# Optimization experiments

Hardware: AMD Instinct MI355X
Metric: run time of the kernel (lower is better)

## Reference

```python
import jax, jax.numpy as jnp
import numpy as np

B, C, H, W = 4, 64, 128, 128
NUM_HEAD = 1
SCALE = (C // NUM_HEAD) ** (-0.5)


def setup_inputs():
    key = jax.random.key(0)
    ks = jax.random.split(key, 32)
    def nrm(k, shape, s=0.05):
        return jax.random.normal(k, shape, jnp.float32) * s
    inp = {"x": jax.random.normal(ks[0], (B, C, H, W), jnp.float32)}
    i = 1
    for wn, bn in [("Wq", "bq"), ("Wk", "bk"), ("Wv", "bv"), ("Wl", "bl"), ("Wo", "bo"), ("Wp", "bp")]:
        inp[wn] = nrm(ks[i], (C, C)); i += 1
        inp[bn] = nrm(ks[i], (C,)); i += 1
    inp["sch_dw"] = nrm(ks[i], (C, 1, 5, 1)); i += 1
    inp["sch_dwb"] = nrm(ks[i], (C,)); i += 1
    inp["sch_pw"] = nrm(ks[i], (C, C, 1, 1)); i += 1
    inp["sch_pwb"] = nrm(ks[i], (C,)); i += 1
    inp["scv_dw"] = nrm(ks[i], (C, 1, 1, 5)); i += 1
    inp["scv_dwb"] = nrm(ks[i], (C,)); i += 1
    inp["scv_pw"] = nrm(ks[i], (C, C, 1, 1)); i += 1
    inp["scv_pwb"] = nrm(ks[i], (C,)); i += 1
    inp["convh_w"] = nrm(ks[i], (C, C, 1, 1)); i += 1
    inp["convh_b"] = nrm(ks[i], (C,)); i += 1
    inp["dsc_dw"] = nrm(ks[i], (C, 1, 3, 3)); i += 1
    inp["dsc_dwb"] = nrm(ks[i], (C,)); i += 1
    inp["dsc_pw"] = nrm(ks[i], (C, C, 1, 1)); i += 1
    inp["dsc_pwb"] = nrm(ks[i], (C,)); i += 1
    inp["ln_g"] = jnp.ones((C,), jnp.float32)
    inp["ln_b"] = jnp.zeros((C,), jnp.float32)
    return inp


def _linear(x, w, b):  # x [B,N,C], w [C,C] (torch Linear convention: y = x @ w.T + b)
    return x @ w.T + b


def _dwconv(x, w, b, pad):  # depthwise: x [B,C,H,W], w [C,1,kh,kw]
    y = jax.lax.conv_general_dilated(x, w, (1, 1), [(pad[0], pad[0]), (pad[1], pad[1])],
                                     dimension_numbers=("NCHW", "OIHW", "NCHW"),
                                     feature_group_count=x.shape[1])
    return y + b[None, :, None, None]


def _pwconv(x, w, b):  # 1x1 conv: w [Co,Ci,1,1]
    return jnp.einsum("bchw,oc->bohw", x, w[:, :, 0, 0]) + b[None, :, None, None]


def _attn(q, k, v):  # [B,N,C] each; dense NxN softmax attention
    a = jax.nn.softmax(jnp.einsum("bnc,bmc->bnm", q, k) * SCALE, axis=-1)
    return jnp.einsum("bnm,bmc->bnc", a, v)


def _up2_bilinear(x):  # bilinear, scale 2, align_corners=True
    Bb, Cc, Hh, Ww = x.shape
    def coords(n):
        s = jnp.linspace(0.0, n - 1.0, 2 * n)
        i0 = jnp.floor(s).astype(jnp.int32)
        i1 = jnp.minimum(i0 + 1, n - 1)
        return i0, i1, (s - i0).astype(x.dtype)
    y0, y1, wy = coords(Hh)
    x0, x1, wx = coords(Ww)
    r = x[:, :, y0, :] * (1.0 - wy)[None, None, :, None] + x[:, :, y1, :] * wy[None, None, :, None]
    return r[:, :, :, x0] * (1.0 - wx) + r[:, :, :, x1] * wx


def _forward(x, Wq, bq, Wk, bk, Wv, bv, Wl, bl, Wo, bo, Wp, bp,
             sch_dw, sch_dwb, sch_pw, sch_pwb, scv_dw, scv_dwb, scv_pw, scv_pwb,
             convh_w, convh_b, dsc_dw, dsc_dwb, dsc_pw, dsc_pwb, ln_g, ln_b):
    Bb, Cc, Hh, Ww = x.shape
    # AvgPool2d(2,2)
    xp = x.reshape(Bb, Cc, Hh // 2, 2, Ww // 2, 2).mean((3, 5))
    Hp, Wp_ = Hh // 2, Ww // 2
    N = Hp * Wp_
    # forward_lpg: GAP-gated self-attention producing low-freq prompt
    gap = xp.mean((2, 3), keepdims=True)
    xg = (gap * xp).reshape(Bb, Cc, N).transpose(0, 2, 1)  # [B,N,C]
    q = _linear(xg, Wq, bq); k = _linear(xg, Wk, bk); v = _linear(xg, Wv, bv)
    prompt_l = _linear(_attn(q, k, v), Wl, bl).transpose(0, 2, 1).reshape(Bb, Cc, Hp, Wp_)
    # forward_hpg: separable strip-conv branches -> high-freq prompt
    x_h = _pwconv(jax.nn.gelu(_dwconv(xp, sch_dw, sch_dwb, (2, 0)), approximate=False), sch_pw, sch_pwb)
    x_v = _pwconv(jax.nn.gelu(_dwconv(xp, scv_dw, scv_dwb, (0, 2)), approximate=False), scv_pw, scv_pwb)
    prompt_h = _pwconv(x_h + x_v, convh_w, convh_b)
    # forward_pgc: cross-attention Q=high, K=low, V=linear(x)
    x_V = _linear(xp.reshape(Bb, Cc, N).transpose(0, 2, 1), Wo, bo)
    x_K = prompt_l.reshape(Bb, Cc, N).transpose(0, 2, 1)
    x_Q = prompt_h.reshape(Bb, Cc, N).transpose(0, 2, 1)
    prompt = _attn(x_Q, x_K, x_V)
    prompt = _linear(prompt, Wp, bp) + x_V
    # LayerNorm over channel dim
    mu = prompt.mean(-1, keepdims=True)
    var = jnp.mean((prompt - mu) ** 2, axis=-1, keepdims=True)
    p_norm = (prompt - mu) / jnp.sqrt(var + 1e-5) * ln_g + ln_b
    p_norm = p_norm.transpose(0, 2, 1).reshape(Bb, Cc, Hp, Wp_)
    # dsc: depthwise 3x3 -> GELU -> 1x1, residual
    out = _pwconv(jax.nn.gelu(_dwconv(p_norm, dsc_dw, dsc_dwb, (1, 1)), approximate=False), dsc_pw, dsc_pwb) + p_norm
    return _up2_bilinear(out)


def reference(x, Wq, bq, Wk, bk, Wv, bv, Wl, bl, Wo, bo, Wp, bp,
              sch_dw, sch_dwb, sch_pw, sch_pwb, scv_dw, scv_dwb, scv_pw, scv_pwb,
              convh_w, convh_b, dsc_dw, dsc_dwb, dsc_pw, dsc_pwb, ln_g, ln_b):
    return _forward(x, Wq, bq, Wk, bk, Wv, bv, Wl, bl, Wo, bo, Wp, bp,
                    sch_dw, sch_dwb, sch_pw, sch_pwb, scv_dw, scv_dwb, scv_pw, scv_pwb,
                    convh_w, convh_b, dsc_dw, dsc_dwb, dsc_pw, dsc_pwb, ln_g, ln_b)
```

## Files before the change

### kernel.cpp

```cpp
#include <hip/hip_runtime.h>
#include <math.h>

#define Bn 4
#define Cn 64
#define Np 4096
#define NSPLIT 4
#define SCALE2 0.18033688011112042f

typedef unsigned short ushort_t;
typedef __attribute__((ext_vector_type(4))) float f32x4;
typedef __attribute__((ext_vector_type(8))) short bf16x8;
typedef __attribute__((ext_vector_type(4))) short bf16x4;

__device__ __forceinline__ float gelu_exact(float x) {
    return 0.5f * x * (1.0f + erff(x * 0.70710678118654752440f));
}
__device__ __forceinline__ ushort_t f2bf(float f) {
    unsigned int u = __float_as_uint(f);
    u += 0x7fffu + ((u >> 16) & 1u);
    return (ushort_t)(u >> 16);
}
__device__ __forceinline__ ushort_t f2bf_tr(float f) {
    return (ushort_t)(__float_as_uint(f) >> 16);
}
__device__ __forceinline__ float bf2f(ushort_t h) {
    return __uint_as_float(((unsigned int)h) << 16);
}
__device__ __forceinline__ void gload_lds16(const ushort_t* g, ushort_t* l) {
    __builtin_amdgcn_global_load_lds(
        (const __attribute__((address_space(1))) void*)g,
        (__attribute__((address_space(3))) void*)l, 16, 0, 0);
}
__device__ __forceinline__ bf16x8 cvt8(const float v[8]) {
    bf16x8 r;
    #pragma unroll
    for (int j = 0; j < 8; ++j) r[j] = (short)f2bf(v[j]);
    return r;
}
__device__ __forceinline__ void gemm16b(const bf16x8 af[2], const ushort_t* __restrict__ Wb,
                                        int l16, int quad, f32x4* acc) {
    #pragma unroll
    for (int cb = 0; cb < 4; ++cb) {
        #pragma unroll
        for (int ks = 0; ks < 2; ++ks) {
            bf16x8 bw = *(const bf16x8*)(Wb + (cb * 16 + l16) * 64 + ks * 32 + quad * 8);
            acc[cb] = __builtin_amdgcn_mfma_f32_16x16x32_bf16(af[ks], bw, acc[cb], 0, 0, 0);
        }
    }
}
__device__ __forceinline__ void gemm16Tb(const bf16x8 af[2], const ushort_t* __restrict__ Wb,
                                         int l16, int quad, f32x4* acc) {
    #pragma unroll
    for (int cb = 0; cb < 4; ++cb) {
        #pragma unroll
        for (int ks = 0; ks < 2; ++ks) {
            bf16x8 bw = *(const bf16x8*)(Wb + (cb * 16 + l16) * 64 + ks * 32 + quad * 8);
            acc[cb] = __builtin_amdgcn_mfma_f32_16x16x32_bf16(bw, af[ks], acc[cb], 0, 0, 0);
        }
    }
}
__device__ __forceinline__ void aload(const float* xs, int row, int quad, bf16x8 af[2]) {
    #pragma unroll
    for (int ks = 0; ks < 2; ++ks) {
        float v[8];
        #pragma unroll
        for (int j = 0; j < 8; ++j) v[j] = xs[(ks * 32 + quad * 8 + j) * 65 + row];
        af[ks] = cvt8(v);
    }
}
__device__ __forceinline__ void stage_bchw(const float* __restrict__ X, int b, int n0, int t,
                                           float* xs) {
    #pragma unroll
    for (int u = 0; u < 16; ++u) {
        int idx = t + u * 256;
        int c = idx >> 6, nl = idx & 63;
        xs[c * 65 + nl] = X[((size_t)(b * Cn + c)) * Np + n0 + nl];
    }
}
__device__ __forceinline__ void stage_comb(const ushort_t* __restrict__ OpB, const float* linv,
                                           int b, int n0, int t, float* xs) {
    const size_t SS = (size_t)Bn * Np * Cn;
    int c4 = (t & 15) * 4;
    #pragma unroll
    for (int u = 0; u < 4; ++u) {
        int nl = (t >> 4) + u * 16;
        size_t gi = ((size_t)(b * Np + n0 + nl)) * Cn + c4;
        ushort4 a0 = *(const ushort4*)(OpB + gi);
        ushort4 a1 = *(const ushort4*)(OpB + SS + gi);
        ushort4 a2 = *(const ushort4*)(OpB + 2 * SS + gi);
        ushort4 a3 = *(const ushort4*)(OpB + 3 * SS + gi);
        float li = linv[nl];
        xs[(c4 + 0) * 65 + nl] = (bf2f(a0.x) + bf2f(a1.x) + bf2f(a2.x) + bf2f(a3.x)) * li;
        xs[(c4 + 1) * 65 + nl] = (bf2f(a0.y) + bf2f(a1.y) + bf2f(a2.y) + bf2f(a3.y)) * li;
        xs[(c4 + 2) * 65 + nl] = (bf2f(a0.z) + bf2f(a1.z) + bf2f(a2.z) + bf2f(a3.z)) * li;
        xs[(c4 + 3) * 65 + nl] = (bf2f(a0.w) + bf2f(a1.w) + bf2f(a2.w) + bf2f(a3.w)) * li;
    }
}
__device__ __forceinline__ void store_bnc_T(ushort_t* __restrict__ Y, int b, int n, int quad,
                                            const f32x4* acc, const float* __restrict__ bias,
                                            float mult) {
    #pragma unroll
    for (int cb = 0; cb < 4; ++cb) {
        int o0 = cb * 16 + quad * 4;
        ushort4 pk;
        pk.x = f2bf((acc[cb][0] + bias[o0 + 0]) * mult);
        pk.y = f2bf((acc[cb][1] + bias[o0 + 1]) * mult);
        pk.z = f2bf((acc[cb][2] + bias[o0 + 2]) * mult);
        pk.w = f2bf((acc[cb][3] + bias[o0 + 3]) * mult);
        *(ushort4*)(Y + ((size_t)(b * Np + n)) * Cn + o0) = pk;
    }
}
__device__ __forceinline__ void store_bchw_bf16(ushort_t* __restrict__ Y, int b, int nb, int l16,
                                                const f32x4* acc, const float* __restrict__ bias) {
    #pragma unroll
    for (int cb = 0; cb < 4; ++cb) {
        int col = cb * 16 + l16;
        float bb = bias[col];
        ushort4 pk;
        pk.x = f2bf(acc[cb][0] + bb); pk.y = f2bf(acc[cb][1] + bb);
        pk.z = f2bf(acc[cb][2] + bb); pk.w = f2bf(acc[cb][3] + bb);
        *(ushort4*)(Y + ((size_t)(b * Cn + col)) * Np + nb) = pk;
    }
}

__global__ void avgpool_kernel(const float* __restrict__ x, float* __restrict__ xp,
                               float* __restrict__ gap4k,
                               const float* __restrict__ convh_w, const float* __restrict__ convh_b,
                               const float* __restrict__ sch_pw, const float* __restrict__ sch_pwb,
                               const float* __restrict__ scv_pw, const float* __restrict__ scv_pwb,
                               ushort_t* __restrict__ Wc1b, ushort_t* __restrict__ Wc2b,
                               float* __restrict__ bcv,
                               const float* __restrict__ Wq, const float* __restrict__ Wk,
                               const float* __restrict__ Wv, const float* __restrict__ Wo,
                               const float* __restrict__ Wl, const float* __restrict__ Wp,
                               const float* __restrict__ dscpw, ushort_t* __restrict__ Wball) {
    if (blockIdx.x < 4096) {
        int idx = blockIdx.x * 256 + threadIdx.x;
        int j  = idx & 63;
        int i  = (idx >> 6) & 63;
        int bc = idx >> 12;
        const float* p = x + ((size_t)bc * 128 + 2 * i) * 128 + 2 * j;
        float v = 0.25f * (p[0] + p[1] + p[128] + p[129]);
        xp[idx] = v;
        float s = v;
        #pragma unroll
        for (int off = 1; off < 64; off <<= 1) s += __shfl_xor(s, off, 64);
        __shared__ float sm[4];
        if ((threadIdx.x & 63) == 0) sm[threadIdx.x >> 6] = s;
        __syncthreads();
        if (threadIdx.x == 0) gap4k[blockIdx.x] = sm[0] + sm[1] + sm[2] + sm[3];
    } else if (blockIdx.x < 4128) {
        int g = (blockIdx.x - 4096) * 256 + threadIdx.x;
        int sel = g >> 12, idx = g & 4095;
        int o = idx >> 6, c = idx & 63;
        const float* pw = sel ? scv_pw : sch_pw;
        float acc = 0.f;
        #pragma unroll 8
        for (int m = 0; m < 64; ++m) acc += convh_w[o * 64 + m] * pw[m * 64 + c];
        (sel ? Wc2b : Wc1b)[idx] = f2bf(acc * SCALE2);
        if (g < 64) {
            float ab = convh_b[g];
            for (int m = 0; m < 64; ++m) ab += convh_w[g * 64 + m] * (sch_pwb[m] + scv_pwb[m]);
            bcv[g] = ab * SCALE2;
        }
    } else {
        int g = (blockIdx.x - 4128) * 256 + threadIdx.x;
        int which = g >> 12, idx = g & 4095;
        const float* srcs[7] = {Wq, Wk, Wv, Wo, Wl, Wp, dscpw};
        Wball[g] = f2bf(srcs[which][idx]);
    }
}

__global__ __launch_bounds__(256) void qkv_dw_kernel(
    const float* __restrict__ xp, const float* __restrict__ gap4k,
    const ushort_t* __restrict__ Wqb, const float* __restrict__ bq,
    const ushort_t* __restrict__ Wkb, const float* __restrict__ bk,
    const ushort_t* __restrict__ Wvb, const float* __restrict__ bv,
    const ushort_t* __restrict__ Wob, const float* __restrict__ bo,
    ushort_t* __restrict__ qb, ushort_t* __restrict__ kb, ushort_t* __restrict__ vb,
    float* __restrict__ xV, ushort_t* __restrict__ xVtb,
    const float* __restrict__ wv5, const float* __restrict__ bv5,
    const float* __restrict__ wh5, const float* __restrict__ bh5,
    ushort_t* __restrict__ gh, ushort_t* __restrict__ gv) {
    int b = blockIdx.y, t = threadIdx.x;
    if (blockIdx.x >= 64) {
        int part = blockIdx.x - 64;
        int e = part * 1024 + t * 4;
        size_t base = (size_t)b * (Cn * Np) + e;
        int c = e >> 12, i = (e >> 6) & 63, j = e & 63;
        const float* p = xp + ((size_t)(b * Cn + c)) * Np;
        float accV[4], accH[4];
        #pragma unroll
        for (int k = 0; k < 4; ++k) { accV[k] = bv5[c]; accH[k] = bh5[c]; }
        #pragma unroll
        for (int d = 0; d < 5; ++d) {
            int ii = i + d - 2;
            if (ii >= 0 && ii < 64) {
                f32x4 r = *(const f32x4*)(p + ii * 64 + j);
                float w = wv5[c * 5 + d];
                accV[0] += w * r[0]; accV[1] += w * r[1];
                accV[2] += w * r[2]; accV[3] += w * r[3];
            }
        }
        f32x4 c0 = *(const f32x4*)(p + i * 64 + j);
        float col[8];
        col[2] = c0[0]; col[3] = c0[1]; col[4] = c0[2]; col[5] = c0[3];
        col[0] = (j >= 2)     ? p[i * 64 + j - 2] : 0.f;
        col[1] = (j >= 1)     ? p[i * 64 + j - 1] : 0.f;
        col[6] = (j + 4 < 64) ? p[i * 64 + j + 4] : 0.f;
        col[7] = (j + 5 < 64) ? p[i * 64 + j + 5] : 0.f;
        #pragma unroll
        for (int k = 0; k < 4; ++k) {
            #pragma unroll
            for (int d = 0; d < 5; ++d) accH[k] += wh5[c * 5 + d] * col[k + d];
        }
        ushort4 ph, pv_;
        ph.x = f2bf(gelu_exact(accV[0])); ph.y = f2bf(gelu_exact(accV[1]));
        ph.z = f2bf(gelu_exact(accV[2])); ph.w = f2bf(gelu_exact(accV[3]));
        pv_.x = f2bf(gelu_exact(accH[0])); pv_.y = f2bf(gelu_exact(accH[1]));
        pv_.z = f2bf(gelu_exact(accH[2])); pv_.w = f2bf(gelu_exact(accH[3]));
        *(ushort4*)(gh + base) = ph;
        *(ushort4*)(gv + base) = pv_;
        return;
    }
    __shared__ float xs[64 * 65];
    __shared__ float gl[64];
    int n0 = blockIdx.x * 64;
    int wv_ = t >> 6, lane = t & 63, l16 = lane & 15, quad = lane >> 4;
    stage_bchw(xp, b, n0, t, xs);
    if (t < 64) {
        float s = 0.f;
        #pragma unroll
        for (int u = 0; u < 16; ++u) s += gap4k[(b * 64 + t) * 16 + u];
        gl[t] = s * (1.f / 4096.f);
    }
    __syncthreads();
    int row = wv_ * 16 + l16;
    int n   = n0 + wv_ * 16 + l16;
    int nb  = n0 + wv_ * 16 + quad * 4;
    bf16x8 ar[2], ag[2];
    #pragma unroll
    for (int ks = 0; ks < 2; ++ks) {
        float vr[8], vg[8];
        #pragma unroll
        for (int j = 0; j < 8; ++j) {
            int k = ks * 32 + quad * 8 + j;
            float xv = xs[k * 65 + row];
            vr[j] = xv; vg[j] = xv * gl[k];
        }
        ar[ks] = cvt8(vr); ag[ks] = cvt8(vg);
    }
    f32x4 acc[4];
    #pragma unroll
    for (int cb = 0; cb < 4; ++cb) acc[cb] = (f32x4){0.f, 0.f, 0.f, 0.f};
    gemm16Tb(ag, Wqb, l16, quad, acc);
    store_bnc_T(qb, b, n, quad, acc, bq, SCALE2);
    #pragma unroll
    for (int cb = 0; cb < 4; ++cb) acc[cb] = (f32x4){0.f, 0.f, 0.f, 0.f};
    gemm16Tb(ag, Wkb, l16, quad, acc);
    store_bnc_T(kb, b, n, quad, acc, bk, 1.f);
    #pragma unroll
    for (int cb = 0; cb < 4; ++cb) acc[cb] = (f32x4){0.f, 0.f, 0.f, 0.f};
    gemm16b(ag, Wvb, l16, quad, acc);
    store_bchw_bf16(vb, b, nb, l16, acc, bv);
    #pragma unroll
    for (int cb = 0; cb < 4; ++cb) acc[cb] = (f32x4){0.f, 0.f, 0.f, 0.f};
    gemm16b(ar, Wob, l16, quad, acc);
    #pragma unroll
    for (int cb = 0; cb < 4; ++cb) {
        int col = cb * 16 + l16;
        float bb = bo[col];
        ushort4 pk;
        float y0 = acc[cb][0] + bb, y1 = acc[cb][1] + bb, y2 = acc[cb][2] + bb, y3 = acc[cb][3] + bb;
        xV[((size_t)(b * Np + nb + 0)) * Cn + col] = y0;
        xV[((size_t)(b * Np + nb + 1)) * Cn + col] = y1;
        xV[((size_t)(b * Np + nb + 2)) * Cn + col] = y2;
        xV[((size_t)(b * Np + nb + 3)) * Cn + col] = y3;
        pk.x = f2bf(y0); pk.y = f2bf(y1); pk.z = f2bf(y2); pk.w = f2bf(y3);
        *(ushort4*)(xVtb + ((size_t)(b * Cn + col)) * Np + nb) = pk;
    }
}

__device__ __forceinline__ void attn_body(
    int xblk, int b, const ushort_t* __restrict__ Qb, const ushort_t* __restrict__ Kb,
    const ushort_t* __restrict__ Vtb, ushort_t* __restrict__ OpB, float* __restrict__ Lpart,
    ushort_t* smem) {
    ushort_t* kt0 = smem;
    ushort_t* vt0 = smem + 8192;
    int split = xblk >> 5;
    int qt    = xblk & 31;
    int n0    = qt * 128;
    int t     = threadIdx.x;
    int wave  = t >> 6, lane = t & 63;
    int l16   = lane & 15, quad = lane >> 4;
    int lrow  = lane >> 3;
    int kvbase = split * (Np / NSPLIT);

    const ushort_t* qp = Qb + ((size_t)(b * Np) + n0 + wave * 32 + l16) * Cn + quad * 8;
    bf16x8 aq00 = *(const bf16x8*)(qp);
    bf16x8 aq01 = *(const bf16x8*)(qp + 32);
    bf16x8 aq10 = *(const bf16x8*)(qp + 16 * Cn);
    bf16x8 aq11 = *(const bf16x8*)(qp + 16 * Cn + 32);

    f32x4 oa0[4], oa1[4];
    float psum0 = 0.f, psum1 = 0.f;
    #pragma unroll
    for (int db = 0; db < 4; ++db) {
        oa0[db] = (f32x4){0.f, 0.f, 0.f, 0.f};
        oa1[db] = (f32x4){0.f, 0.f, 0.f, 0.f};
    }

    int wh  = wave & 1;
    int jsw = ((lane & 7) ^ lrow) & 7;
    const ushort_t* gK  = Kb + ((size_t)b * Np + kvbase + wh * 32 + lrow) * Cn + jsw * 8;
    const ushort_t* gV0 = Vtb + ((size_t)(b * Cn) + wh * 32 + lrow) * Np + kvbase + jsw * 8;
    const ushort_t* gV1 = gV0 + (size_t)8 * Np;
    const ushort_t* gV2 = gV0 + (size_t)16 * Np;
    const ushort_t* gV3 = gV0 + (size_t)24 * Np;
    ushort_t* ldK = kt0 + wh * 2048;
    ushort_t* ldV = vt0 + wh * 2048;

    const ushort_t* kr0 = kt0 + l16 * 64 + ((quad ^ (l16 & 7)) & 7) * 8;
    const ushort_t* kr1 = kt0 + l16 * 64 + (((quad + 4) ^ (l16 & 7)) & 7) * 8;
    int h = quad >> 1, q1 = quad & 1, e = l16 & 7;
    const ushort_t* vr0 = vt0 + l16 * 64 + (((0 + h) ^ e) & 7) * 8 + q1 * 4;
    const ushort_t* vr1 = vt0 + l16 * 64 + (((2 + h) ^ e) & 7) * 8 + q1 * 4;
    const ushort_t* vr2 = vt0 + l16 * 64 + (((4 + h) ^ e) & 7) * 8 + q1 * 4;
    const ushort_t* vr3 = vt0 + l16 * 64 + (((6 + h) ^ e) & 7) * 8 + q1 * 4;

    auto stage = [&](int buf) {
        if (wave < 2) {
            ushort_t* dst = ldK + buf * 4096;
            gload_lds16(gK,        dst);
            gload_lds16(gK + 512,  dst + 512);
            gload_lds16(gK + 1024, dst + 1024);
            gload_lds16(gK + 1536, dst + 1536);
            gK += 64 * Cn;
        } else {
            ushort_t* dst = ldV + buf * 4096;
            gload_lds16(gV0, dst);
            gload_lds16(gV1, dst + 512);
            gload_lds16(gV2, dst + 1024);
            gload_lds16(gV3, dst + 1536);
            gV0 += 64; gV1 += 64; gV2 += 64; gV3 += 64;
        }
    };

    auto compute = [&](int B2) {
        const int ko = B2 * 4096;
        f32x4 sa0[4], sa1[4];
        #pragma unroll
        for (int cb = 0; cb < 4; ++cb) {
            sa0[cb] = (f32x4){0.f, 0.f, 0.f, 0.f};
            sa1[cb] = (f32x4){0.f, 0.f, 0.f, 0.f};
        }
        #pragma unroll
        for (int cb = 0; cb < 4; ++cb) {
            bf16x8 bk0 = *(const bf16x8*)(kr0 + ko + cb * 1024);
            bf16x8 bk1 = *(const bf16x8*)(kr1 + ko + cb * 1024);
            sa0[cb] = __builtin_amdgcn_mfma_f32_16x16x32_bf16(bk0, aq00, sa0[cb], 0, 0, 0);
            sa0[cb] = __builtin_amdgcn_mfma_f32_16x16x32_bf16(bk1, aq01, sa0[cb], 0, 0, 0);
            sa1[cb] = __builtin_amdgcn_mfma_f32_16x16x32_bf16(bk0, aq10, sa1[cb], 0, 0, 0);
            sa1[cb] = __builtin_amdgcn_mfma_f32_16x16x32_bf16(bk1, aq11, sa1[cb], 0, 0, 0);
        }
        bf16x4 pb0[4], pb1[4];
        #pragma unroll
        for (int cb = 0; cb < 4; ++cb) {
            float p0 = exp2f(sa0[cb][0]), p1 = exp2f(sa0[cb][1]);
            float p2 = exp2f(sa0[cb][2]), p3 = exp2f(sa0[cb][3]);
            psum0 += (p0 + p1) + (p2 + p3);
            bf16x4 pk;
            pk[0] = (short)f2bf_tr(p0); pk[1] = (short)f2bf_tr(p1);
            pk[2] = (short)f2bf_tr(p2); pk[3] = (short)f2bf_tr(p3);
            pb0[cb] = pk;
            float q0 = exp2f(sa1[cb][0]), q1f = exp2f(sa1[cb][1]);
            float q2 = exp2f(sa1[cb][2]), q3 = exp2f(sa1[cb][3]);
            psum1 += (q0 + q1f) + (q2 + q3);
            bf16x4 qk;
            qk[0] = (short)f2bf_tr(q0); qk[1] = (short)f2bf_tr(q1f);
            qk[2] = (short)f2bf_tr(q2); qk[3] = (short)f2bf_tr(q3);
            pb1[cb] = qk;
        }
        #pragma unroll
        for (int db = 0; db < 4; ++db) {
            bf16x4 a0 = *(const bf16x4*)(vr0 + ko + db * 1024);
            bf16x4 a1 = *(const bf16x4*)(vr1 + ko + db * 1024);
            bf16x4 a2 = *(const bf16x4*)(vr2 + ko + db * 1024);
            bf16x4 a3 = *(const bf16x4*)(vr3 + ko + db * 1024);
            oa0[db] = __builtin_amdgcn_mfma_f32_16x16x16bf16_1k(a0, pb0[0], oa0[db], 0, 0, 0);
            oa0[db] = __builtin_amdgcn_mfma_f32_16x16x16bf16_1k(a1, pb0[1], oa0[db], 0, 0, 0);
            oa0[db] = __builtin_amdgcn_mfma_f32_16x16x16bf16_1k(a2, pb0[2], oa0[db], 0, 0, 0);
            oa0[db] = __builtin_amdgcn_mfma_f32_16x16x16bf16_1k(a3, pb0[3], oa0[db], 0, 0, 0);
            oa1[db] = __builtin_amdgcn_mfma_f32_16x16x16bf16_1k(a0, pb1[0], oa1[db], 0, 0, 0);
            oa1[db] = __builtin_amdgcn_mfma_f32_16x16x16bf16_1k(a1, pb1[1], oa1[db], 0, 0, 0);
            oa1[db] = __builtin_amdgcn_mfma_f32_16x16x16bf16_1k(a2, pb1[2], oa1[db], 0, 0, 0);
            oa1[db] = __builtin_amdgcn_mfma_f32_16x16x16bf16_1k(a3, pb1[3], oa1[db], 0, 0, 0);
        }
        __syncthreads();
    };

    const int NT = (Np / NSPLIT) / 64;
    stage(0);
    __syncthreads();
    #pragma unroll 1
    for (int mm = 0; mm < NT / 2; ++mm) {
        stage(1);
        compute(0);
        if (mm < NT / 2 - 1) stage(0);
        compute(1);
    }

    psum0 += __shfl_xor(psum0, 16, 64);
    psum0 += __shfl_xor(psum0, 32, 64);
    psum1 += __shfl_xor(psum1, 16, 64);
    psum1 += __shfl_xor(psum1, 32, 64);
    size_t obase = ((size_t)(split * Bn + b)) * Np;
    int n = n0 + wave * 32 + l16;
    if (quad == 0) {
        Lpart[obase + n]      = psum0;
        Lpart[obase + n + 16] = psum1;
    }
    #pragma unroll
    for (int db = 0; db < 4; ++db) {
        ushort4 pk;
        pk.x = f2bf(oa0[db][0]); pk.y = f2bf(oa0[db][1]);
        pk.z = f2bf(oa0[db][2]); pk.w = f2bf(oa0[db][3]);
        *(ushort4*)(OpB + (obase + n) * Cn + db * 16 + quad * 4) = pk;
        ushort4 qk;
        qk.x = f2bf(oa1[db][0]); qk.y = f2bf(oa1[db][1]);
        qk.z = f2bf(oa1[db][2]); qk.w = f2bf(oa1[db][3]);
        *(ushort4*)(OpB + (obase + n + 16) * Cn + db * 16 + quad * 4) = qk;
    }
}

__device__ __forceinline__ void hpg_body(
    int tile, int b, const ushort_t* __restrict__ gh, const ushort_t* __restrict__ gv,
    const ushort_t* __restrict__ Wc1b, const ushort_t* __restrict__ Wc2b,
    const float* __restrict__ bcv,
    ushort_t* __restrict__ xQb, ushort_t* smem) {
    ushort_t* xs1 = smem;
    ushort_t* xs2 = smem + 4608;
    int n0 = tile * 64, t = threadIdx.x;
    int wv_ = t >> 6, lane = t & 63, l16 = lane & 15, quad = lane >> 4;
    #pragma unroll
    for (int u = 0; u < 4; ++u) {
        int lin = u * 256 + t;
        int c = lin >> 4, nl4 = (lin & 15) * 4;
        size_t gi = ((size_t)(b * Cn + c)) * Np + n0 + nl4;
        ushort4 g1 = *(const ushort4*)(gh + gi);
        ushort4 g2 = *(const ushort4*)(gv + gi);
        xs1[(nl4 + 0) * 72 + c] = g1.x; xs1[(nl4 + 1) * 72 + c] = g1.y;
        xs1[(nl4 + 2) * 72 + c] = g1.z; xs1[(nl4 + 3) * 72 + c] = g1.w;
        xs2[(nl4 + 0) * 72 + c] = g2.x; xs2[(nl4 + 1) * 72 + c] = g2.y;
        xs2[(nl4 + 2) * 72 + c] = g2.z; xs2[(nl4 + 3) * 72 + c] = g2.w;
    }
    __syncthreads();
    int row = wv_ * 16 + l16;
    bf16x8 a1[2], a2[2];
    #pragma unroll
    for (int ks = 0; ks < 2; ++ks) {
        a1[ks] = *(const bf16x8*)(xs1 + row * 72 + ks * 32 + quad * 8);
        a2[ks] = *(const bf16x8*)(xs2 + row * 72 + ks * 32 + quad * 8);
    }
    f32x4 acc[4];
    #pragma unroll
    for (int cb = 0; cb < 4; ++cb) acc[cb] = (f32x4){0.f, 0.f, 0.f, 0.f};
    gemm16Tb(a1, Wc1b, l16, quad, acc);
    gemm16Tb(a2, Wc2b, l16, quad, acc);
    store_bnc_T(xQb, b, n0 + wv_ * 16 + l16, quad, acc, bcv, 1.f);
}

__global__ __launch_bounds__(256) void attn_hpg_kernel(
    const ushort_t* __restrict__ Qb, const ushort_t* __restrict__ Kb,
    const ushort_t* __restrict__ Vtb, ushort_t* __restrict__ OpB, float* __restrict__ Lpart,
    const ushort_t* __restrict__ gh, const ushort_t* __restrict__ gv,
    const ushort_t* __restrict__ Wc1b, const ushort_t* __restrict__ Wc2b,
    const float* __restrict__ bcv, ushort_t* __restrict__ xQb) {
    __shared__ ushort_t smem[16384];
    int b = blockIdx.y;
    if (blockIdx.x < 128)
        attn_body(blockIdx.x, b, Qb, Kb, Vtb, OpB, Lpart, smem);
    else
        hpg_body(blockIdx.x - 128, b, gh, gv, Wc1b, Wc2b, bcv, xQb, smem);
}

__global__ __launch_bounds__(256) void wl_mfma(
    const ushort_t* __restrict__ OpB, const float* __restrict__ Lp,
    const ushort_t* __restrict__ Wlb, const float* __restrict__ bl, ushort_t* __restrict__ xKb) {
    __shared__ float xs[64 * 65];
    __shared__ float linv[64];
    int b = blockIdx.y, n0 = blockIdx.x * 64, t = threadIdx.x;
    int wv_ = t >> 6, lane = t & 63, l16 = lane & 15, quad = lane >> 4;
    if (t < 64) {
        size_t li = (size_t)b * Np + n0 + t;
        const size_t LS = (size_t)Bn * Np;
        linv[t] = 1.f / (Lp[li] + Lp[LS + li] + Lp[2 * LS + li] + Lp[3 * LS + li]);
    }
    __syncthreads();
    stage_comb(OpB, linv, b, n0, t, xs);
    __syncthreads();
    bf16x8 af[2];
    aload(xs, wv_ * 16 + l16, quad, af);
    f32x4 acc[4];
    #pragma unroll
    for (int cb = 0; cb < 4; ++cb) acc[cb] = (f32x4){0.f, 0.f, 0.f, 0.f};
    gemm16Tb(af, Wlb, l16, quad, acc);
    store_bnc_T(xKb, b, n0 + wv_ * 16 + l16, quad, acc, bl, 1.f);
}

__global__ __launch_bounds__(256) void linln_mfma(
    const ushort_t* __restrict__ OpB, const float* __restrict__ Lp,
    const ushort_t* __restrict__ Wpb, const float* __restrict__ bp,
    const float* __restrict__ xV, const float* __restrict__ g, const float* __restrict__ beta,
    float* __restrict__ out) {
    __shared__ float xs[64 * 65];
    __shared__ float linv[64];
    int b = blockIdx.y, n0 = blockIdx.x * 64, t = threadIdx.x;
    int wv_ = t >> 6, lane = t & 63, l16 = lane & 15, quad = lane >> 4;
    if (t < 64) {
        size_t li = (size_t)b * Np + n0 + t;
        const size_t LS = (size_t)Bn * Np;
        linv[t] = 1.f / (Lp[li] + Lp[LS + li] + Lp[2 * LS + li] + Lp[3 * LS + li]);
    }
    __syncthreads();
    stage_comb(OpB, linv, b, n0, t, xs);
    __syncthreads();
    bf16x8 af[2];
    aload(xs, wv_ * 16 + l16, quad, af);
    f32x4 acc[4];
    #pragma unroll
    for (int cb = 0; cb < 4; ++cb) acc[cb] = (f32x4){0.f, 0.f, 0.f, 0.f};
    gemm16b(af, Wpb, l16, quad, acc);
    int nb = n0 + wv_ * 16 + quad * 4;
    float vals[4][4], gc[4], bec[4];
    #pragma unroll
    for (int cb = 0; cb < 4; ++cb) {
        int col = cb * 16 + l16;
        float bb = bp[col];
        gc[cb] = g[col]; bec[cb] = beta[col];
        #pragma unroll
        for (int r = 0; r < 4; ++r)
            vals[cb][r] = acc[cb][r] + bb + xV[((size_t)(b * Np + nb + r)) * Cn + col];
    }
    f32x4 yn[4];
    #pragma unroll
    for (int r = 0; r < 4; ++r) {
        float s = 0.f, s2 = 0.f;
        #pragma unroll
        for (int cb = 0; cb < 4; ++cb) { s += vals[cb][r]; s2 += vals[cb][r] * vals[cb][r]; }
        #pragma unroll
        for (int off = 1; off < 16; off <<= 1) {
            s  += __shfl_xor(s, off, 64);
            s2 += __shfl_xor(s2, off, 64);
        }
        float mu  = s * (1.f / 64.f);
        float var = s2 * (1.f / 64.f) - mu * mu;
        float ivs = rsqrtf(var + 1e-5f);
        #pragma unroll
        for (int cb = 0; cb < 4; ++cb)
            yn[cb][r] = (vals[cb][r] - mu) * ivs * gc[cb] + bec[cb];
    }
    #pragma unroll
    for (int cb = 0; cb < 4; ++cb)
        *(f32x4*)(out + ((size_t)(b * Cn + cb * 16 + l16)) * Np + nb) = yn[cb];
}

__global__ __launch_bounds__(256) void dsc_mfma(
    const float* __restrict__ X, const float* __restrict__ dw, const float* __restrict__ dwb,
    const ushort_t* __restrict__ Wb, const float* __restrict__ bias, float* __restrict__ out) {
    __shared__ float xs[64 * 65];
    int b = blockIdx.y, irow = blockIdx.x, n0 = irow * 64, t = threadIdx.x;
    int wv_ = t >> 6, lane = t & 63, l16 = lane & 15, quad = lane >> 4;
    int j = t & 63;
    #pragma unroll
    for (int u = 0; u < 16; ++u) {
        int c = (t >> 6) + u * 4;
        const float* p = X + ((size_t)(b * Cn + c)) * Np + n0;
        float acc = dwb[c];
        #pragma unroll
        for (int dy = 0; dy < 3; ++dy) {
            int ii = irow + dy - 1;
            if (ii < 0 || ii >= 64) continue;
            const float* pr = p + (dy - 1) * 64;
            #pragma unroll
            for (int dx = 0; dx < 3; ++dx) {
                int jj = j + dx - 1;
                if (jj < 0 || jj >= 64) continue;
                acc += dw[c * 9 + dy * 3 + dx] * pr[jj];
            }
        }
        xs[c * 65 + j] = gelu_exact(acc);
    }
    __syncthreads();
    bf16x8 af[2];
    aload(xs, wv_ * 16 + l16, quad, af);
    f32x4 acc[4];
    #pragma unroll
    for (int cb = 0; cb < 4; ++cb) acc[cb] = (f32x4){0.f, 0.f, 0.f, 0.f};
    gemm16b(af, Wb, l16, quad, acc);
    int nb = n0 + wv_ * 16 + quad * 4;
    #pragma unroll
    for (int cb = 0; cb < 4; ++cb) {
        int col = cb * 16 + l16;
        float bb = bias[col];
        size_t oi = ((size_t)(b * Cn + col)) * Np + nb;
        f32x4 rv = *(const f32x4*)(X + oi);
        f32x4 v4;
        #pragma unroll
        for (int r = 0; r < 4; ++r) v4[r] = acc[cb][r] + bb + rv[r];
        *(f32x4*)(out + oi) = v4;
    }
}

__global__ void upsample_kernel(const float* __restrict__ in, float* __restrict__ out) {
    int idx = blockIdx.x * 256 + threadIdx.x;
    int x4 = (idx & 31) * 4;
    int y  = (idx >> 5) & 127;
    int bc = idx >> 12;
    float sy = y * (63.f / 127.f);
    int y0 = (int)sy;
    float fy = sy - y0;
    int y1 = min(y0 + 1, 63);
    const float* p0 = in + (size_t)bc * Np + y0 * 64;
    const float* p1 = in + (size_t)bc * Np + y1 * 64;
    f32x4 o;
    #pragma unroll
    for (int k = 0; k < 4; ++k) {
        int xo = x4 + k;
        float sx = xo * (63.f / 127.f);
        int x0 = (int)sx;
        float fx = sx - x0;
        int x1 = min(x0 + 1, 63);
        float r0 = p0[x0] + (p0[x1] - p0[x0]) * fx;
        float r1 = p1[x0] + (p1[x1] - p1[x0]) * fx;
        o[k] = r0 + (r1 - r0) * fy;
    }
    *(f32x4*)(out + (size_t)idx * 4) = o;
}

extern "C" void kernel_launch(void* const* d_in, const int* in_sizes, int n_in,
                              void* d_out, int out_size, void* d_ws, size_t ws_size,
                              hipStream_t stream) {
    const float* x       = (const float*)d_in[0];
    const float* Wq      = (const float*)d_in[1];
    const float* bq      = (const float*)d_in[2];
    const float* Wk      = (const float*)d_in[3];
    const float* bk      = (const float*)d_in[4];
    const float* Wv      = (const float*)d_in[5];
    const float* bv      = (const float*)d_in[6];
    const float* Wl      = (const float*)d_in[7];
    const float* bl      = (const float*)d_in[8];
    const float* Wo      = (const float*)d_in[9];
    const float* bo      = (const float*)d_in[10];
    const float* Wp      = (const float*)d_in[11];
    const float* bp      = (const float*)d_in[12];
    const float* sch_dw  = (const float*)d_in[13];
    const float* sch_dwb = (const float*)d_in[14];
    const float* sch_pw  = (const float*)d_in[15];
    const float* sch_pwb = (const float*)d_in[16];
    const float* scv_dw  = (const float*)d_in[17];
    const float* scv_dwb = (const float*)d_in[18];
    const float* scv_pw  = (const float*)d_in[19];
    const float* scv_pwb = (const float*)d_in[20];
    const float* convh_w = (const float*)d_in[21];
    const float* convh_b = (const float*)d_in[22];
    const float* dsc_dw  = (const float*)d_in[23];
    const float* dsc_dwb = (const float*)d_in[24];
    const float* dsc_pw  = (const float*)d_in[25];
    const float* dsc_pwb = (const float*)d_in[26];
    const float* ln_g    = (const float*)d_in[27];
    const float* ln_b    = (const float*)d_in[28];

    float* ws = (float*)d_ws;
    const size_t SZ = (size_t)Bn * Np * Cn;
    float* xp   = ws;
    float* xV   = ws + SZ;
    ushort_t* ghb = (ushort_t*)(ws + 2 * SZ);
    ushort_t* gh  = ghb;
    ushort_t* gv  = ghb + SZ;
    float* f2   = ws + 2 * SZ;
    ushort_t* bws  = (ushort_t*)(ws + 3 * SZ);
    ushort_t* qb   = bws;
    ushort_t* kb_  = bws + SZ;
    ushort_t* vb   = bws + 2 * SZ;
    ushort_t* xKb  = bws + 3 * SZ;
    ushort_t* xVtb = bws + 4 * SZ;
    ushort_t* xQb  = bws + 5 * SZ;
    ushort_t* OpB  = (ushort_t*)(ws + 6 * SZ);
    float* gap4k  = ws + 8 * SZ;
    float* Lpart  = gap4k + 4096;
    float* wcslot = Lpart + (size_t)NSPLIT * Bn * Np;
    ushort_t* Wc1b = (ushort_t*)wcslot;
    ushort_t* Wc2b = Wc1b + 4096;
    float* bcv  = wcslot + 4096;
    ushort_t* Wball = (ushort_t*)(bcv + 64);
    ushort_t* Wqb   = Wball;
    ushort_t* Wkb   = Wball + 4096;
    ushort_t* Wvb   = Wball + 8192;
    ushort_t* Wob   = Wball + 12288;
    ushort_t* Wlb   = Wball + 16384;
    ushort_t* Wpb   = Wball + 20480;
    ushort_t* Wdscb = Wball + 24576;

    dim3 g64(64, Bn);

    avgpool_kernel<<<4096 + 32 + 112, 256, 0, stream>>>(x, xp, gap4k,
                                                  convh_w, convh_b, sch_pw, sch_pwb,
                                                  scv_pw, scv_pwb, Wc1b, Wc2b, bcv,
                                                  Wq, Wk, Wv, Wo, Wl, Wp, dsc_pw, Wball);
    qkv_dw_kernel<<<dim3(64 + 256, Bn), 256, 0, stream>>>(
        xp, gap4k, Wqb, bq, Wkb, bk, Wvb, bv, Wob, bo,
        qb, kb_, vb, xV, xVtb, sch_dw, sch_dwb, scv_dw, scv_dwb, gh, gv);
    attn_hpg_kernel<<<dim3(128 + 64, Bn), 256, 0, stream>>>(
        qb, kb_, vb, OpB, Lpart, gh, gv, Wc1b, Wc2b, bcv, xQb);
    wl_mfma<<<g64, 256, 0, stream>>>(OpB, Lpart, Wlb, bl, xKb);
    attn_hpg_kernel<<<dim3(128, Bn), 256, 0, stream>>>(
        xQb, xKb, xVtb, OpB, Lpart, gh, gv, Wc1b, Wc2b, bcv, xQb);
    linln_mfma<<<g64, 256, 0, stream>>>(OpB, Lpart, Wpb, bp, xV, ln_g, ln_b, xp);
    dsc_mfma<<<g64, 256, 0, stream>>>(xp, dsc_dw, dsc_dwb, Wdscb, dsc_pwb, f2);
    upsample_kernel<<<4096, 256, 0, stream>>>(f2, (float*)d_out);
}
```

Before: 264.0 us.

## Load attention K/V tiles directly from global memory into registers, dropping LDS staging

The attention body no longer double-buffers K and V tiles through shared memory with global_load_lds and block barriers. Each wave now loads its MFMA operands straight from global memory into registers, relying on cache reuse across waves, and the shared array shrinks to what the other branch needs. It also raises wave priority around the MFMA blocks with s_setprio. Removing the barriers and LDS traffic may help occupancy and latency, but every wave now issues redundant global loads of the same K/V data, which risks L2 bandwidth pressure.

New measurement: 364.5 us. 1.38x slower.

```diff
diff --git a/kernel.cpp b/kernel.cpp
--- a/kernel.cpp
+++ b/kernel.cpp
@@ -25,11 +25,6 @@
 }
 __device__ __forceinline__ float bf2f(ushort_t h) {
     return __uint_as_float(((unsigned int)h) << 16);
-}
-__device__ __forceinline__ void gload_lds16(const ushort_t* g, ushort_t* l) {
-    __builtin_amdgcn_global_load_lds(
-        (const __attribute__((address_space(1))) void*)g,
-        (__attribute__((address_space(3))) void*)l, 16, 0, 0);
 }
 __device__ __forceinline__ bf16x8 cvt8(const float v[8]) {
     bf16x8 r;
@@ -283,17 +278,13 @@
 
 __device__ __forceinline__ void attn_body(
     int xblk, int b, const ushort_t* __restrict__ Qb, const ushort_t* __restrict__ Kb,
-    const ushort_t* __restrict__ Vtb, ushort_t* __restrict__ OpB, float* __restrict__ Lpart,
-    ushort_t* smem) {
-    ushort_t* kt0 = smem;
-    ushort_t* vt0 = smem + 8192;
+    const ushort_t* __restrict__ Vtb, ushort_t* __restrict__ OpB, float* __restrict__ Lpart) {
     int split = xblk >> 5;
     int qt    = xblk & 31;
     int n0    = qt * 128;
     int t     = threadIdx.x;
     int wave  = t >> 6, lane = t & 63;
     int l16   = lane & 15, quad = lane >> 4;
-    int lrow  = lane >> 3;
     int kvbase = split * (Np / NSPLIT);
 
     const ushort_t* qp = Qb + ((size_t)(b * Np) + n0 + wave * 32 + l16) * Cn + quad * 8;
@@ -310,59 +301,44 @@
         oa1[db] = (f32x4){0.f, 0.f, 0.f, 0.f};
     }
 
-    int wh  = wave & 1;
-    int jsw = ((lane & 7) ^ lrow) & 7;
-    const ushort_t* gK  = Kb + ((size_t)b * Np + kvbase + wh * 32 + lrow) * Cn + jsw * 8;
-    const ushort_t* gV0 = Vtb + ((size_t)(b * Cn) + wh * 32 + lrow) * Np + kvbase + jsw * 8;
-    const ushort_t* gV1 = gV0 + (size_t)8 * Np;
-    const ushort_t* gV2 = gV0 + (size_t)16 * Np;
-    const ushort_t* gV3 = gV0 + (size_t)24 * Np;
-    ushort_t* ldK = kt0 + wh * 2048;
-    ushort_t* ldV = vt0 + wh * 2048;
-
-    const ushort_t* kr0 = kt0 + l16 * 64 + ((quad ^ (l16 & 7)) & 7) * 8;
-    const ushort_t* kr1 = kt0 + l16 * 64 + (((quad + 4) ^ (l16 & 7)) & 7) * 8;
-    int h = quad >> 1, q1 = quad & 1, e = l16 & 7;
-    const ushort_t* vr0 = vt0 + l16 * 64 + (((0 + h) ^ e) & 7) * 8 + q1 * 4;
-    const ushort_t* vr1 = vt0 + l16 * 64 + (((2 + h) ^ e) & 7) * 8 + q1 * 4;
-    const ushort_t* vr2 = vt0 + l16 * 64 + (((4 + h) ^ e) & 7) * 8 + q1 * 4;
-    const ushort_t* vr3 = vt0 + l16 * 64 + (((6 + h) ^ e) & 7) * 8 + q1 * 4;
-
-    auto stage = [&](int buf) {
-        if (wave < 2) {
-            ushort_t* dst = ldK + buf * 4096;
-            gload_lds16(gK,        dst);
-            gload_lds16(gK + 512,  dst + 512);
-            gload_lds16(gK + 1024, dst + 1024);
-            gload_lds16(gK + 1536, dst + 1536);
-            gK += 64 * Cn;
-        } else {
-            ushort_t* dst = ldV + buf * 4096;
-            gload_lds16(gV0, dst);
-            gload_lds16(gV1, dst + 512);
-            gload_lds16(gV2, dst + 1024);
-            gload_lds16(gV3, dst + 1536);
-            gV0 += 64; gV1 += 64; gV2 += 64; gV3 += 64;
-        }
-    };
-
-    auto compute = [&](int B2) {
-        const int ko = B2 * 4096;
+    const ushort_t* kp = Kb + ((size_t)b * Np + kvbase + l16) * Cn + quad * 8;
+    const ushort_t* vp0 = Vtb + ((size_t)(b * Cn) + l16) * Np + kvbase + quad * 4;
+    const ushort_t* vp1 = vp0 + (size_t)16 * Np;
+    const ushort_t* vp2 = vp0 + (size_t)32 * Np;
+    const ushort_t* vp3 = vp0 + (size_t)48 * Np;
+
+    const int NT = (Np / NSPLIT) / 64;
+    #pragma unroll 2
+    for (int m = 0; m < NT; ++m) {
+        bf16x8 bk[4][2];
+        #pragma unroll
+        for (int cb = 0; cb < 4; ++cb) {
+            bk[cb][0] = *(const bf16x8*)(kp + cb * 1024);
+            bk[cb][1] = *(const bf16x8*)(kp + cb * 1024 + 32);
+        }
+        bf16x4 av[4][4];
+        #pragma unroll
+        for (int kc = 0; kc < 4; ++kc) {
+            av[kc][0] = *(const bf16x4*)(vp0 + kc * 16);
+            av[kc][1] = *(const bf16x4*)(vp1 + kc * 16);
+            av[kc][2] = *(const bf16x4*)(vp2 + kc * 16);
+            av[kc][3] = *(const bf16x4*)(vp3 + kc * 16);
+        }
         f32x4 sa0[4], sa1[4];
         #pragma unroll
         for (int cb = 0; cb < 4; ++cb) {
             sa0[cb] = (f32x4){0.f, 0.f, 0.f, 0.f};
             sa1[cb] = (f32x4){0.f, 0.f, 0.f, 0.f};
         }
+        __builtin_amdgcn_s_setprio(1);
         #pragma unroll
         for (int cb = 0; cb < 4; ++cb) {
-            bf16x8 bk0 = *(const bf16x8*)(kr0 + ko + cb * 1024);
-            bf16x8 bk1 = *(const bf16x8*)(kr1 + ko + cb * 1024);
-            sa0[cb] = __builtin_amdgcn_mfma_f32_16x16x32_bf16(bk0, aq00, sa0[cb], 0, 0, 0);
-            sa0[cb] = __builtin_amdgcn_mfma_f32_16x16x32_bf16(bk1, aq01, sa0[cb], 0, 0, 0);
-            sa1[cb] = __builtin_amdgcn_mfma_f32_16x16x32_bf16(bk0, aq10, sa1[cb], 0, 0, 0);
-            sa1[cb] = __builtin_amdgcn_mfma_f32_16x16x32_bf16(bk1, aq11, sa1[cb], 0, 0, 0);
-        }
+            sa0[cb] = __builtin_amdgcn_mfma_f32_16x16x32_bf16(bk[cb][0], aq00, sa0[cb], 0, 0, 0);
+            sa0[cb] = __builtin_amdgcn_mfma_f32_16x16x32_bf16(bk[cb][1], aq01, sa0[cb], 0, 0, 0);
+            sa1[cb] = __builtin_amdgcn_mfma_f32_16x16x32_bf16(bk[cb][0], aq10, sa1[cb], 0, 0, 0);
+            sa1[cb] = __builtin_amdgcn_mfma_f32_16x16x32_bf16(bk[cb][1], aq11, sa1[cb], 0, 0, 0);
+        }
+        __builtin_amdgcn_s_setprio(0);
         bf16x4 pb0[4], pb1[4];
         #pragma unroll
         for (int cb = 0; cb < 4; ++cb) {
@@ -381,33 +357,18 @@
             qk[2] = (short)f2bf_tr(q2); qk[3] = (short)f2bf_tr(q3);
             pb1[cb] = qk;
         }
+        __builtin_amdgcn_s_setprio(1);
         #pragma unroll
         for (int db = 0; db < 4; ++db) {
-            bf16x4 a0 = *(const bf16x4*)(vr0 + ko + db * 1024);
-            bf16x4 a1 = *(const bf16x4*)(vr1 + ko + db * 1024);
-            bf16x4 a2 = *(const bf16x4*)(vr2 + ko + db * 1024);
-            bf16x4 a3 = *(const bf16x4*)(vr3 + ko + db * 1024);
-            oa0[db] = __builtin_amdgcn_mfma_f32_16x16x16bf16_1k(a0, pb0[0], oa0[db], 0, 0, 0);
-            oa0[db] = __builtin_amdgcn_mfma_f32_16x16x16bf16_1k(a1, pb0[1], oa0[db], 0, 0, 0);
-            oa0[db] = __builtin_amdgcn_mfma_f32_16x16x16bf16_1k(a2, pb0[2], oa0[db], 0, 0, 0);
-            oa0[db] = __builtin_amdgcn_mfma_f32_16x16x16bf16_1k(a3, pb0[3], oa0[db], 0, 0, 0);
-            oa1[db] = __builtin_amdgcn_mfma_f32_16x16x16bf16_1k(a0, pb1[0], oa1[db], 0, 0, 0);
-            oa1[db] = __builtin_amdgcn_mfma_f32_16x16x16bf16_1k(a1, pb1[1], oa1[db], 0, 0, 0);
-            oa1[db] = __builtin_amdgcn_mfma_f32_16x16x16bf16_1k(a2, pb1[2], oa1[db], 0, 0, 0);
-            oa1[db] = __builtin_amdgcn_mfma_f32_16x16x16bf16_1k(a3, pb1[3], oa1[db], 0, 0, 0);
-        }
-        __syncthreads();
-    };
-
-    const int NT = (Np / NSPLIT) / 64;
-    stage(0);
-    __syncthreads();
-    #pragma unroll 1
-    for (int mm = 0; mm < NT / 2; ++mm) {
-        stage(1);
-        compute(0);
-        if (mm < NT / 2 - 1) stage(0);
-        compute(1);
+            #pragma unroll
+            for (int kc = 0; kc < 4; ++kc) {
+                oa0[db] = __builtin_amdgcn_mfma_f32_16x16x16bf16_1k(av[kc][db], pb0[kc], oa0[db], 0, 0, 0);
+                oa1[db] = __builtin_amdgcn_mfma_f32_16x16x16bf16_1k(av[kc][db], pb1[kc], oa1[db], 0, 0, 0);
+            }
+        }
+        __builtin_amdgcn_s_setprio(0);
+        kp  += 64 * Cn;
+        vp0 += 64; vp1 += 64; vp2 += 64; vp3 += 64;
     }
 
     psum0 += __shfl_xor(psum0, 16, 64);
@@ -476,10 +437,10 @@
     const ushort_t* __restrict__ gh, const ushort_t* __restrict__ gv,
     const ushort_t* __restrict__ Wc1b, const ushort_t* __restrict__ Wc2b,
     const float* __restrict__ bcv, ushort_t* __restrict__ xQb) {
-    __shared__ ushort_t smem[16384];
+    __shared__ ushort_t smem[9216];
     int b = blockIdx.y;
     if (blockIdx.x < 128)
-        attn_body(blockIdx.x, b, Qb, Kb, Vtb, OpB, Lpart, smem);
+        attn_body(blockIdx.x, b, Qb, Kb, Vtb, OpB, Lpart);
     else
         hpg_body(blockIdx.x - 128, b, gh, gv, Wc1b, Wc2b, bcv, xQb, smem);
 }
```
